# Kernel tuning notes

Measured on AMD Instinct MI355X. Metric: run time of the kernel, lower is better.

Reference implementation:

```python
import jax, jax.numpy as jnp
import numpy as np


def setup_inputs() -> dict:
    key = jax.random.key(0)
    k1, k2, k3 = jax.random.split(key, 3)
    B, N, M = 8, 4096, 4096
    recon = jax.random.normal(k1, (B, M, 3), dtype=jnp.float32)
    src_points = jax.random.normal(k2, (B, N, 3), dtype=jnp.float32)
    transform = jax.random.normal(k3, (B, 4, 4), dtype=jnp.float32)
    return {"recon": recon, "src_points": src_points, "transform": transform}


def _apply_transform(points, transform):
    # points: [B,N,3], transform: [B,4,4] -> p @ R^T + t
    R = transform[:, :3, :3]   # [B,3,3]
    t = transform[:, :3, 3]    # [B,3]
    return jnp.einsum('bnd,bkd->bnk', points, R) + t[:, None, :]


def reference(recon, src_points, transform):
    gts = _apply_transform(src_points, transform)  # [B,N,3]
    preds = recon                                   # [B,M,3]
    # pairwise squared distances P[b,i,j] = |gts_i|^2 + |preds_j|^2 - 2 gts_i . preds_j
    xx = jnp.sum(gts * gts, axis=-1)                # [B,N]
    yy = jnp.sum(preds * preds, axis=-1)            # [B,M]
    zz = jnp.einsum('bnd,bmd->bnm', gts, preds)     # [B,N,M]
    P = xx[:, :, None] + yy[:, None, :] - 2.0 * zz  # [B,N,M]
    loss_1 = jnp.sum(jnp.min(P, axis=1))            # min over gts for each pred
    loss_2 = jnp.sum(jnp.min(P, axis=2))            # min over preds for each gt
    return loss_1 + loss_2
```

## Files before the change

### kernel.cpp

```cpp
#include <hip/hip_runtime.h>
#include <math.h>

#define TPB       256
#define KA        16
#define QPB       (TPB * KA)
#define C_CHUNKS  32
#define CPTS      128
#define CHUNK_F   (CPTS * 4)

typedef float v2f __attribute__((ext_vector_type(2)));

__global__ __launch_bounds__(TPB) void prep_kernel(
    const float* __restrict__ recon,
    const float* __restrict__ src,
    const float* __restrict__ T,
    float* __restrict__ preds_soa,
    float* __restrict__ gts_soa,
    float* __restrict__ out, int out_n,
    int B, int N, int M)
{
    int idx = blockIdx.x * TPB + threadIdx.x;
    if (idx < out_n) out[idx] = 0.0f;
    int totG = B * N;
    int totP = B * M;
    if (idx < totG) {
        int b = idx / N, n = idx - b * N;
        const float* Tb = T + b * 16;
        float x = src[3*idx + 0], y = src[3*idx + 1], z = src[3*idx + 2];
        float gx = fmaf(Tb[0], x, fmaf(Tb[1], y, fmaf(Tb[2],  z, Tb[3])));
        float gy = fmaf(Tb[4], x, fmaf(Tb[5], y, fmaf(Tb[6],  z, Tb[7])));
        float gz = fmaf(Tb[8], x, fmaf(Tb[9], y, fmaf(Tb[10], z, Tb[11])));
        size_t base = ((size_t)b * (N / CPTS) + (n >> 7)) * CHUNK_F + (n & 127);
        gts_soa[base      ] = gx;
        gts_soa[base + 128] = gy;
        gts_soa[base + 256] = gz;
        gts_soa[base + 384] = fmaf(gx, gx, fmaf(gy, gy, gz * gz));
    } else if (idx - totG < totP) {
        int k = idx - totG;
        int b = k / M, m = k - b * M;
        float x = recon[3*k + 0], y = recon[3*k + 1], z = recon[3*k + 2];
        size_t base = ((size_t)b * (M / CPTS) + (m >> 7)) * CHUNK_F + (m & 127);
        preds_soa[base      ] = x;
        preds_soa[base + 128] = y;
        preds_soa[base + 256] = z;
        preds_soa[base + 384] = fmaf(x, x, fmaf(y, y, z * z));
    }
}

__global__ __launch_bounds__(TPB, 2) void chamfer_kernel(
    const float* __restrict__ gts_soa,
    const float* __restrict__ preds_soa,
    float* __restrict__ partial,
    int B, int N, int M, int GQ)
{
    __shared__ __align__(16) float sL[CHUNK_F];

    const int dir = blockIdx.z;
    const int b   = blockIdx.y;
    const int c   = blockIdx.x;

    const int NA  = (dir == 0) ? N : M;
    const int NB_ = (dir == 0) ? M : N;

    const float* __restrict__ Asoa = (dir == 0) ? gts_soa : preds_soa;
    const float* __restrict__ Bsoa = (dir == 0) ? preds_soa : gts_soa;
    const int gq_base = ((dir == 0) ? 0 : B * N) + b * NA;

    {
        const float4* gsrc = (const float4*)(Bsoa + ((size_t)b * (NB_ / CPTS) + c) * CHUNK_F);
        if (threadIdx.x < CPTS) ((float4*)sL)[threadIdx.x] = gsrc[threadIdx.x];
    }
    __syncthreads();

    float aw[KA], mA[KA], mB[KA];
    v2f A2X[KA], A2Y[KA], A2Z[KA];
    const int qi0 = (int)threadIdx.x;
    #pragma unroll
    for (int k = 0; k < KA; ++k) {
        int q = qi0 + k * TPB;
        const float* ab = Asoa + ((size_t)b * (NA / CPTS) + (q >> 7)) * CHUNK_F + (q & 127);
        float ax = ab[0], ay = ab[128], az = ab[256];
        aw[k] = ab[384];
        float tx = -2.0f * ax, ty = -2.0f * ay, tz = -2.0f * az;
        A2X[k].x = tx; A2X[k].y = tx;
        A2Y[k].x = ty; A2Y[k].y = ty;
        A2Z[k].x = tz; A2Z[k].y = tz;
        mA[k] = INFINITY; mB[k] = INFINITY;
    }

    const v2f* sX = (const v2f*)(sL +   0);
    const v2f* sY = (const v2f*)(sL + 128);
    const v2f* sZ = (const v2f*)(sL + 256);
    const v2f* sW = (const v2f*)(sL + 384);

    for (int jj = 0; jj < CPTS / 2; jj += 2) {
        v2f x0 = sX[jj],   y0 = sY[jj],   z0 = sZ[jj],   w0 = sW[jj];
        v2f x1 = sX[jj+1], y1 = sY[jj+1], z1 = sZ[jj+1], w1 = sW[jj+1];
        #pragma unroll
        for (int k = 0; k < KA; ++k) {
            v2f d0, d1;
            asm("v_pk_fma_f32 %0, %1, %2, %3" : "=v"(d0) : "v"(A2Z[k]), "v"(z0), "v"(w0));
            asm("v_pk_fma_f32 %0, %1, %2, %0" : "+v"(d0) : "v"(A2Y[k]), "v"(y0));
            asm("v_pk_fma_f32 %0, %1, %2, %0" : "+v"(d0) : "v"(A2X[k]), "v"(x0));
            asm("v_pk_fma_f32 %0, %1, %2, %3" : "=v"(d1) : "v"(A2Z[k]), "v"(z1), "v"(w1));
            asm("v_pk_fma_f32 %0, %1, %2, %0" : "+v"(d1) : "v"(A2Y[k]), "v"(y1));
            asm("v_pk_fma_f32 %0, %1, %2, %0" : "+v"(d1) : "v"(A2X[k]), "v"(x1));
            mA[k] = fminf(fminf(mA[k], d0.x), d0.y);
            mB[k] = fminf(fminf(mB[k], d1.x), d1.y);
        }
    }

    #pragma unroll
    for (int k = 0; k < KA; ++k) {
        int q = qi0 + k * TPB;
        partial[(size_t)c * GQ + gq_base + q] = aw[k] + fminf(mA[k], mB[k]);
    }
}

__global__ __launch_bounds__(TPB) void reduce_kernel(
    const float* __restrict__ partial, float* __restrict__ out, int GQ)
{
    int q = blockIdx.x * TPB + threadIdx.x;
    float m = 0.0f;
    if (q < GQ) {
        m = partial[q];
        #pragma unroll
        for (int c = 1; c < C_CHUNKS; ++c)
            m = fminf(m, partial[(size_t)c * GQ + q]);
    }
    #pragma unroll
    for (int off = 32; off > 0; off >>= 1) m += __shfl_down(m, off);
    __shared__ float red[TPB / 64];
    if ((threadIdx.x & 63) == 0) red[threadIdx.x >> 6] = m;
    __syncthreads();
    if (threadIdx.x == 0) {
        float s = 0.0f;
        #pragma unroll
        for (int w = 0; w < TPB / 64; ++w) s += red[w];
        atomicAdd(out, s);
    }
}

extern "C" void kernel_launch(void* const* d_in, const int* in_sizes, int n_in,
                              void* d_out, int out_size, void* d_ws, size_t ws_size,
                              hipStream_t stream)
{
    const float* recon = (const float*)d_in[0];
    const float* src   = (const float*)d_in[1];
    const float* T     = (const float*)d_in[2];

    const int B = in_sizes[2] / 16;
    const int M = in_sizes[0] / (B * 3);
    const int N = in_sizes[1] / (B * 3);
    const int GQ = B * (N + M);

    float* preds_soa = (float*)d_ws;
    float* gts_soa   = preds_soa + (size_t)B * M * 4;
    float* partial   = gts_soa + (size_t)B * N * 4;
    float* out       = (float*)d_out;

    prep_kernel<<<dim3((GQ + TPB - 1) / TPB), dim3(TPB), 0, stream>>>(
        recon, src, T, preds_soa, gts_soa, out, out_size, B, N, M);

    dim3 grid(C_CHUNKS, B, 2);
    chamfer_kernel<<<grid, dim3(TPB), 0, stream>>>(gts_soa, preds_soa, partial, B, N, M, GQ);

    reduce_kernel<<<dim3((GQ + TPB - 1) / TPB), dim3(TPB), 0, stream>>>(partial, out, GQ);
}
```

Measured before the change: 88.05 us.

## Use AoS float4 points, smaller chunks with more blocks, and v_min3 reductions

Prep now writes one packed float4 per point instead of the chunked SoA layout. The chamfer kernel splits each batch's B-side points into 64 chunks of 64 instead of 32 of 128, doubling the grid, and raises the launch_bounds occupancy hint to 4 blocks. Shared memory is transposed into SoA at load time, and the running min uses v_min3_f32 so two min ops become one. The aim is more parallelism and fewer VALU ops, at the cost of twice the partial-min traffic and a longer reduce loop.

```diff
diff --git a/kernel.cpp b/kernel.cpp
--- a/kernel.cpp
+++ b/kernel.cpp
@@ -3,9 +3,8 @@
 
 #define TPB       256
 #define KA        16
-#define QPB       (TPB * KA)
-#define C_CHUNKS  32
-#define CPTS      128
+#define C_CHUNKS  64
+#define CPTS      64
 #define CHUNK_F   (CPTS * 4)
 
 typedef float v2f __attribute__((ext_vector_type(2)));
@@ -14,8 +13,7 @@
     const float* __restrict__ recon,
     const float* __restrict__ src,
     const float* __restrict__ T,
-    float* __restrict__ preds_soa,
-    float* __restrict__ gts_soa,
+    float4* __restrict__ qarr,
     float* __restrict__ out, int out_n,
     int B, int N, int M)
 {
@@ -24,32 +22,22 @@
     int totG = B * N;
     int totP = B * M;
     if (idx < totG) {
-        int b = idx / N, n = idx - b * N;
+        int b = idx / N;
         const float* Tb = T + b * 16;
         float x = src[3*idx + 0], y = src[3*idx + 1], z = src[3*idx + 2];
         float gx = fmaf(Tb[0], x, fmaf(Tb[1], y, fmaf(Tb[2],  z, Tb[3])));
         float gy = fmaf(Tb[4], x, fmaf(Tb[5], y, fmaf(Tb[6],  z, Tb[7])));
         float gz = fmaf(Tb[8], x, fmaf(Tb[9], y, fmaf(Tb[10], z, Tb[11])));
-        size_t base = ((size_t)b * (N / CPTS) + (n >> 7)) * CHUNK_F + (n & 127);
-        gts_soa[base      ] = gx;
-        gts_soa[base + 128] = gy;
-        gts_soa[base + 256] = gz;
-        gts_soa[base + 384] = fmaf(gx, gx, fmaf(gy, gy, gz * gz));
+        qarr[idx] = make_float4(gx, gy, gz, fmaf(gx, gx, fmaf(gy, gy, gz * gz)));
     } else if (idx - totG < totP) {
         int k = idx - totG;
-        int b = k / M, m = k - b * M;
         float x = recon[3*k + 0], y = recon[3*k + 1], z = recon[3*k + 2];
-        size_t base = ((size_t)b * (M / CPTS) + (m >> 7)) * CHUNK_F + (m & 127);
-        preds_soa[base      ] = x;
-        preds_soa[base + 128] = y;
-        preds_soa[base + 256] = z;
-        preds_soa[base + 384] = fmaf(x, x, fmaf(y, y, z * z));
+        qarr[totG + k] = make_float4(x, y, z, fmaf(x, x, fmaf(y, y, z * z)));
     }
 }
 
-__global__ __launch_bounds__(TPB, 2) void chamfer_kernel(
-    const float* __restrict__ gts_soa,
-    const float* __restrict__ preds_soa,
+__global__ __launch_bounds__(TPB, 4) void chamfer_kernel(
+    const float4* __restrict__ qarr,
     float* __restrict__ partial,
     int B, int N, int M, int GQ)
 {
@@ -59,39 +47,37 @@
     const int b   = blockIdx.y;
     const int c   = blockIdx.x;
 
-    const int NA  = (dir == 0) ? N : M;
-    const int NB_ = (dir == 0) ? M : N;
+    const int NA    = (dir == 0) ? N : M;
+    const int Abase = (dir == 0) ? b * N : B * N + b * M;
+    const int Bbase = (dir == 0) ? B * N + b * M : b * N;
 
-    const float* __restrict__ Asoa = (dir == 0) ? gts_soa : preds_soa;
-    const float* __restrict__ Bsoa = (dir == 0) ? preds_soa : gts_soa;
-    const int gq_base = ((dir == 0) ? 0 : B * N) + b * NA;
-
-    {
-        const float4* gsrc = (const float4*)(Bsoa + ((size_t)b * (NB_ / CPTS) + c) * CHUNK_F);
-        if (threadIdx.x < CPTS) ((float4*)sL)[threadIdx.x] = gsrc[threadIdx.x];
+    if (threadIdx.x < CPTS) {
+        float4 p = qarr[Bbase + c * CPTS + (int)threadIdx.x];
+        sL[threadIdx.x           ] = p.x;
+        sL[threadIdx.x + CPTS    ] = p.y;
+        sL[threadIdx.x + CPTS * 2] = p.z;
+        sL[threadIdx.x + CPTS * 3] = p.w;
     }
     __syncthreads();
 
     float aw[KA], mA[KA], mB[KA];
     v2f A2X[KA], A2Y[KA], A2Z[KA];
-    const int qi0 = (int)threadIdx.x;
     #pragma unroll
     for (int k = 0; k < KA; ++k) {
-        int q = qi0 + k * TPB;
-        const float* ab = Asoa + ((size_t)b * (NA / CPTS) + (q >> 7)) * CHUNK_F + (q & 127);
-        float ax = ab[0], ay = ab[128], az = ab[256];
-        aw[k] = ab[384];
-        float tx = -2.0f * ax, ty = -2.0f * ay, tz = -2.0f * az;
+        int q = (int)threadIdx.x + k * TPB;
+        float4 a = qarr[Abase + q];
+        aw[k] = a.w;
+        float tx = -2.0f * a.x, ty = -2.0f * a.y, tz = -2.0f * a.z;
         A2X[k].x = tx; A2X[k].y = tx;
         A2Y[k].x = ty; A2Y[k].y = ty;
         A2Z[k].x = tz; A2Z[k].y = tz;
         mA[k] = INFINITY; mB[k] = INFINITY;
     }
 
-    const v2f* sX = (const v2f*)(sL +   0);
-    const v2f* sY = (const v2f*)(sL + 128);
-    const v2f* sZ = (const v2f*)(sL + 256);
-    const v2f* sW = (const v2f*)(sL + 384);
+    const v2f* sX = (const v2f*)(sL);
+    const v2f* sY = (const v2f*)(sL + CPTS);
+    const v2f* sZ = (const v2f*)(sL + CPTS * 2);
+    const v2f* sW = (const v2f*)(sL + CPTS * 3);
 
     for (int jj = 0; jj < CPTS / 2; jj += 2) {
         v2f x0 = sX[jj],   y0 = sY[jj],   z0 = sZ[jj],   w0 = sW[jj];
@@ -105,15 +91,15 @@
             asm("v_pk_fma_f32 %0, %1, %2, %3" : "=v"(d1) : "v"(A2Z[k]), "v"(z1), "v"(w1));
             asm("v_pk_fma_f32 %0, %1, %2, %0" : "+v"(d1) : "v"(A2Y[k]), "v"(y1));
             asm("v_pk_fma_f32 %0, %1, %2, %0" : "+v"(d1) : "v"(A2X[k]), "v"(x1));
-            mA[k] = fminf(fminf(mA[k], d0.x), d0.y);
-            mB[k] = fminf(fminf(mB[k], d1.x), d1.y);
+            asm("v_min3_f32 %0, %0, %1, %2" : "+v"(mA[k]) : "v"(d0.x), "v"(d0.y));
+            asm("v_min3_f32 %0, %0, %1, %2" : "+v"(mB[k]) : "v"(d1.x), "v"(d1.y));
         }
     }
 
     #pragma unroll
     for (int k = 0; k < KA; ++k) {
-        int q = qi0 + k * TPB;
-        partial[(size_t)c * GQ + gq_base + q] = aw[k] + fminf(mA[k], mB[k]);
+        int q = (int)threadIdx.x + k * TPB;
+        partial[(size_t)c * GQ + Abase + q] = aw[k] + fminf(mA[k], mB[k]);
     }
 }
 
@@ -124,7 +110,7 @@
     float m = 0.0f;
     if (q < GQ) {
         m = partial[q];
-        #pragma unroll
+        #pragma unroll 7
         for (int c = 1; c < C_CHUNKS; ++c)
             m = fminf(m, partial[(size_t)c * GQ + q]);
     }
@@ -154,16 +140,15 @@
     const int N = in_sizes[1] / (B * 3);
     const int GQ = B * (N + M);
 
-    float* preds_soa = (float*)d_ws;
-    float* gts_soa   = preds_soa + (size_t)B * M * 4;
-    float* partial   = gts_soa + (size_t)B * N * 4;
-    float* out       = (float*)d_out;
+    float4* qarr    = (float4*)d_ws;
+    float*  partial = (float*)(qarr + GQ);
+    float*  out     = (float*)d_out;
 
     prep_kernel<<<dim3((GQ + TPB - 1) / TPB), dim3(TPB), 0, stream>>>(
-        recon, src, T, preds_soa, gts_soa, out, out_size, B, N, M);
+        recon, src, T, qarr, out, out_size, B, N, M);
 
     dim3 grid(C_CHUNKS, B, 2);
-    chamfer_kernel<<<grid, dim3(TPB), 0, stream>>>(gts_soa, preds_soa, partial, B, N, M, GQ);
+    chamfer_kernel<<<grid, dim3(TPB), 0, stream>>>(qarr, partial, B, N, M, GQ);
 
     reduce_kernel<<<dim3((GQ + TPB - 1) / TPB), dim3(TPB), 0, stream>>>(partial, out, GQ);
 }
```

New measurement: 144.8 us. +64.5%, slower.
